# Performance work log

Measured on AMD Instinct MI355X. Metric: run time of the kernel, lower is better.

Reference implementation:

```python
import jax, jax.numpy as jnp
import numpy as np

KNN_K = 3  # module hard-codes top-3 farthest sememes (torch.sort descending)


def setup_inputs() -> dict:
    key = jax.random.key(0)
    k1, k2, k3 = jax.random.split(key, 3)
    V, H = 50257, 1024
    L, W, S = 256, 16, 32
    embedding = jax.random.normal(k1, (V, H), dtype=jnp.float32)
    word_ids = jax.random.randint(k2, (L, W), 0, V, dtype=jnp.int32)
    sememe_ids = jax.random.randint(k3, (L, W, S), 0, V, dtype=jnp.int32)
    return {"embedding": embedding, "word_ids": word_ids, "sememe_ids": sememe_ids}


def reference(embedding, word_ids, sememe_ids):
    # embedding: [V,H]; word_ids: [L,W]; sememe_ids: [L,W,S]
    w = embedding[word_ids]                  # [L,W,H]  word embeddings (s)
    sm = embedding[sememe_ids]               # [L,W,S,H] sememe embeddings
    # F.pairwise_distance(s, sememe_tensor, p=2): L2 per sememe
    dist = jnp.linalg.norm(sm - w[:, :, None, :], axis=-1)  # [L,W,S]
    # torch.sort(distance, descending=True)[1][:3] -> 3 farthest sememes
    _, idx = jax.lax.top_k(dist, KNN_K)                      # [L,W,K]
    sel = jnp.take_along_axis(sm, idx[..., None], axis=2)    # [L,W,K,H]
    # cat([knn_mean.unsqueeze(0), s], 0).mean(0) == (knn_mean + s) / 2
    per_word = 0.5 * (sel.mean(axis=2) + w)                  # [L,W,H]
    # stack(span).mean(0): mean over words in each label
    return per_word.mean(axis=1)                             # [L,H]
```

## Files before the change

### kernel.cpp

```cpp
#include <hip/hip_runtime.h>


#define HDIM 1024
#define SNUM 32
#define WNUM 16
#define KNN  3

__global__ __launch_bounds__(256) void knn_dist_kernel(
    const float* __restrict__ emb,
    const int*   __restrict__ word_ids,
    const int*   __restrict__ sem_ids,
    float*       __restrict__ dist_part,
    int nj)
{
    const int wave = threadIdx.x >> 6;
    const int lane = threadIdx.x & 63;
    const int blk  = blockIdx.x;
    const int b    = blk >> 2;
    const int quarter = blk & 3;

    const int base_s = b * SNUM + wave * 8;
    const int col    = quarter * 256 + 4 * lane;

    const int4 sa = *(const int4*)(sem_ids + base_s);
    const int4 sb = *(const int4*)(sem_ids + base_s + 4);
    const int  wid = word_ids[b];

    const float4 w = *(const float4*)(emb + (size_t)wid * HDIM + col);

    const int sids[8] = {sa.x, sa.y, sa.z, sa.w, sb.x, sb.y, sb.z, sb.w};
    float4 sv[8];
    #pragma unroll
    for (int k = 0; k < 8; ++k)
        sv[k] = *(const float4*)(emb + (size_t)sids[k] * HDIM + col);

    #pragma unroll
    for (int k = 0; k < 8; ++k) {
        const float dx = sv[k].x - w.x;
        const float dy = sv[k].y - w.y;
        const float dz = sv[k].z - w.z;
        const float dw = sv[k].w - w.w;
        float d = (dx * dx + dy * dy) + (dz * dz + dw * dw);
        #pragma unroll
        for (int off = 32; off >= 1; off >>= 1)
            d += __shfl_xor(d, off, 64);
        if (lane == 0)
            dist_part[(size_t)quarter * nj + base_s + k] = d;
    }
}

__global__ __launch_bounds__(256) void knn_select_kernel(
    const float* __restrict__ dist_part,
    const int*   __restrict__ word_ids,
    const int*   __restrict__ sem_ids,
    int*         __restrict__ sel,
    int nb, int nj)
{
    const int b = blockIdx.x * 256 + threadIdx.x;
    if (b >= nb) return;

    float4 acc[8];
    #pragma unroll
    for (int i = 0; i < 8; ++i) acc[i] = make_float4(0.f, 0.f, 0.f, 0.f);

    #pragma unroll
    for (int q = 0; q < 4; ++q) {
        const float4* p = (const float4*)(dist_part + (size_t)q * nj + b * SNUM);
        #pragma unroll
        for (int i = 0; i < 8; ++i) {
            const float4 v = p[i];
            acc[i].x += v.x; acc[i].y += v.y; acc[i].z += v.z; acc[i].w += v.w;
        }
    }

    float dl[SNUM];
    #pragma unroll
    for (int i = 0; i < 8; ++i) {
        dl[4 * i + 0] = acc[i].x;
        dl[4 * i + 1] = acc[i].y;
        dl[4 * i + 2] = acc[i].z;
        dl[4 * i + 3] = acc[i].w;
    }

    unsigned chosen = 0;
    #pragma unroll
    for (int k = 0; k < KNN; ++k) {
        float best = -1.0f;
        int   bi   = 0;
        #pragma unroll
        for (int s = 0; s < SNUM; ++s) {
            if (!((chosen >> s) & 1u) && dl[s] > best) { best = dl[s]; bi = s; }
        }
        chosen |= (1u << bi);
        sel[b * 4 + k] = sem_ids[b * SNUM + bi];
    }
    sel[b * 4 + 3] = word_ids[b];
}

__global__ __launch_bounds__(256) void knn_out_kernel(
    const float* __restrict__ emb,
    const int*   __restrict__ sel,
    float*       __restrict__ out)
{
    const int l = blockIdx.x >> 2;
    const int q = blockIdx.x & 3;
    const int h = q * 256 + threadIdx.x;

    __shared__ int s_ids[WNUM * 4];
    if (threadIdx.x < WNUM * 4) s_ids[threadIdx.x] = sel[l * WNUM * 4 + threadIdx.x];
    __syncthreads();

    const float third = 1.0f / 3.0f;
    float acc = 0.0f;
    #pragma unroll
    for (int w = 0; w < WNUM; ++w) {
        const float e0 = emb[(size_t)s_ids[w * 4 + 0] * HDIM + h];
        const float e1 = emb[(size_t)s_ids[w * 4 + 1] * HDIM + h];
        const float e2 = emb[(size_t)s_ids[w * 4 + 2] * HDIM + h];
        const float ew = emb[(size_t)s_ids[w * 4 + 3] * HDIM + h];
        acc += (e0 + e1 + e2) * third + ew;
    }
    out[(size_t)l * HDIM + h] = acc * (0.5f / 16.0f);
}

extern "C" void kernel_launch(void* const* d_in, const int* in_sizes, int n_in,
                              void* d_out, int out_size, void* d_ws, size_t ws_size,
                              hipStream_t stream) {
    const float* emb  = (const float*)d_in[0];
    const int*   wids = (const int*)d_in[1];
    const int*   sids = (const int*)d_in[2];
    float*       out  = (float*)d_out;

    const int nb = in_sizes[1];
    const int nj = in_sizes[2];
    const int L  = out_size / HDIM;

    float* dist_part = (float*)d_ws;
    int*   sel       = (int*)((char*)d_ws + (size_t)4 * nj * 4);

    knn_dist_kernel<<<dim3(nb * 4), dim3(256), 0, stream>>>(emb, wids, sids, dist_part, nj);
    knn_select_kernel<<<dim3((nb + 255) / 256), dim3(256), 0, stream>>>(dist_part, wids, sids, sel, nb, nj);
    knn_out_kernel<<<dim3(L * 4), dim3(256), 0, stream>>>(emb, sel, out);
}
```

Baseline: 91.57 us.

## Fuse top-k selection into output kernel and vectorize gathers and distance stores

Result: no change. 90.18 us (-1.5%).

```diff
diff --git a/kernel.cpp b/kernel.cpp
--- a/kernel.cpp
+++ b/kernel.cpp
@@ -19,14 +19,19 @@
     const int b    = blk >> 2;
     const int quarter = blk & 3;
 
+    __shared__ float s_w[256];
+
+    const int wid = word_ids[b];
+    s_w[threadIdx.x] = emb[(size_t)wid * HDIM + quarter * 256 + threadIdx.x];
+
     const int base_s = b * SNUM + wave * 8;
     const int col    = quarter * 256 + 4 * lane;
 
     const int4 sa = *(const int4*)(sem_ids + base_s);
     const int4 sb = *(const int4*)(sem_ids + base_s + 4);
-    const int  wid = word_ids[b];
 
-    const float4 w = *(const float4*)(emb + (size_t)wid * HDIM + col);
+    __syncthreads();
+    const float4 w = *(const float4*)(s_w + 4 * lane);
 
     const int sids[8] = {sa.x, sa.y, sa.z, sa.w, sb.x, sb.y, sb.z, sb.w};
     float4 sv[8];
@@ -34,93 +39,97 @@
     for (int k = 0; k < 8; ++k)
         sv[k] = *(const float4*)(emb + (size_t)sids[k] * HDIM + col);
 
+    float d[8];
     #pragma unroll
     for (int k = 0; k < 8; ++k) {
         const float dx = sv[k].x - w.x;
         const float dy = sv[k].y - w.y;
         const float dz = sv[k].z - w.z;
         const float dw = sv[k].w - w.w;
-        float d = (dx * dx + dy * dy) + (dz * dz + dw * dw);
+        d[k] = (dx * dx + dy * dy) + (dz * dz + dw * dw);
+    }
+
+    #pragma unroll
+    for (int k = 0; k < 8; ++k) {
         #pragma unroll
         for (int off = 32; off >= 1; off >>= 1)
-            d += __shfl_xor(d, off, 64);
-        if (lane == 0)
-            dist_part[(size_t)quarter * nj + base_s + k] = d;
+            d[k] += __shfl_xor(d[k], off, 64);
+    }
+
+    if (lane == 0) {
+        float* p = dist_part + (size_t)quarter * nj + base_s;
+        *(float4*)(p + 0) = make_float4(d[0], d[1], d[2], d[3]);
+        *(float4*)(p + 4) = make_float4(d[4], d[5], d[6], d[7]);
     }
 }
 
-__global__ __launch_bounds__(256) void knn_select_kernel(
+__global__ __launch_bounds__(256) void knn_outsel_kernel(
+    const float* __restrict__ emb,
     const float* __restrict__ dist_part,
     const int*   __restrict__ word_ids,
     const int*   __restrict__ sem_ids,
-    int*         __restrict__ sel,
-    int nb, int nj)
+    float*       __restrict__ out,
+    int nj)
 {
-    const int b = blockIdx.x * 256 + threadIdx.x;
-    if (b >= nb) return;
+    const int l = blockIdx.x;
+    const int t = threadIdx.x;
 
-    float4 acc[8];
-    #pragma unroll
-    for (int i = 0; i < 8; ++i) acc[i] = make_float4(0.f, 0.f, 0.f, 0.f);
+    __shared__ int s_ids[WNUM * 4];
 
-    #pragma unroll
-    for (int q = 0; q < 4; ++q) {
-        const float4* p = (const float4*)(dist_part + (size_t)q * nj + b * SNUM);
+    if (t < WNUM) {
+        const int b = l * WNUM + t;
+        float4 acc[8];
+        #pragma unroll
+        for (int i = 0; i < 8; ++i) acc[i] = make_float4(0.f, 0.f, 0.f, 0.f);
+        #pragma unroll
+        for (int q = 0; q < 4; ++q) {
+            const float4* p = (const float4*)(dist_part + (size_t)q * nj + b * SNUM);
+            #pragma unroll
+            for (int i = 0; i < 8; ++i) {
+                const float4 v = p[i];
+                acc[i].x += v.x; acc[i].y += v.y; acc[i].z += v.z; acc[i].w += v.w;
+            }
+        }
+        float dl[SNUM];
         #pragma unroll
         for (int i = 0; i < 8; ++i) {
-            const float4 v = p[i];
-            acc[i].x += v.x; acc[i].y += v.y; acc[i].z += v.z; acc[i].w += v.w;
+            dl[4 * i + 0] = acc[i].x;
+            dl[4 * i + 1] = acc[i].y;
+            dl[4 * i + 2] = acc[i].z;
+            dl[4 * i + 3] = acc[i].w;
         }
+        unsigned chosen = 0;
+        #pragma unroll
+        for (int k = 0; k < KNN; ++k) {
+            float best = -1.0f;
+            int   bi   = 0;
+            #pragma unroll
+            for (int s = 0; s < SNUM; ++s) {
+                if (!((chosen >> s) & 1u) && dl[s] > best) { best = dl[s]; bi = s; }
+            }
+            chosen |= (1u << bi);
+            s_ids[t * 4 + k] = sem_ids[b * SNUM + bi];
+        }
+        s_ids[t * 4 + 3] = word_ids[b];
     }
-
-    float dl[SNUM];
-    #pragma unroll
-    for (int i = 0; i < 8; ++i) {
-        dl[4 * i + 0] = acc[i].x;
-        dl[4 * i + 1] = acc[i].y;
-        dl[4 * i + 2] = acc[i].z;
-        dl[4 * i + 3] = acc[i].w;
-    }
-
-    unsigned chosen = 0;
-    #pragma unroll
-    for (int k = 0; k < KNN; ++k) {
-        float best = -1.0f;
-        int   bi   = 0;
-        #pragma unroll
-        for (int s = 0; s < SNUM; ++s) {
-            if (!((chosen >> s) & 1u) && dl[s] > best) { best = dl[s]; bi = s; }
-        }
-        chosen |= (1u << bi);
-        sel[b * 4 + k] = sem_ids[b * SNUM + bi];
-    }
-    sel[b * 4 + 3] = word_ids[b];
-}
-
-__global__ __launch_bounds__(256) void knn_out_kernel(
-    const float* __restrict__ emb,
-    const int*   __restrict__ sel,
-    float*       __restrict__ out)
-{
-    const int l = blockIdx.x >> 2;
-    const int q = blockIdx.x & 3;
-    const int h = q * 256 + threadIdx.x;
-
-    __shared__ int s_ids[WNUM * 4];
-    if (threadIdx.x < WNUM * 4) s_ids[threadIdx.x] = sel[l * WNUM * 4 + threadIdx.x];
     __syncthreads();
 
     const float third = 1.0f / 3.0f;
-    float acc = 0.0f;
-    #pragma unroll
+    float ax = 0.f, ay = 0.f, az = 0.f, aw = 0.f;
+    #pragma unroll 4
     for (int w = 0; w < WNUM; ++w) {
-        const float e0 = emb[(size_t)s_ids[w * 4 + 0] * HDIM + h];
-        const float e1 = emb[(size_t)s_ids[w * 4 + 1] * HDIM + h];
-        const float e2 = emb[(size_t)s_ids[w * 4 + 2] * HDIM + h];
-        const float ew = emb[(size_t)s_ids[w * 4 + 3] * HDIM + h];
-        acc += (e0 + e1 + e2) * third + ew;
+        const float4 e0 = *(const float4*)(emb + (size_t)s_ids[w * 4 + 0] * HDIM + 4 * t);
+        const float4 e1 = *(const float4*)(emb + (size_t)s_ids[w * 4 + 1] * HDIM + 4 * t);
+        const float4 e2 = *(const float4*)(emb + (size_t)s_ids[w * 4 + 2] * HDIM + 4 * t);
+        const float4 ew = *(const float4*)(emb + (size_t)s_ids[w * 4 + 3] * HDIM + 4 * t);
+        ax += (e0.x + e1.x + e2.x) * third + ew.x;
+        ay += (e0.y + e1.y + e2.y) * third + ew.y;
+        az += (e0.z + e1.z + e2.z) * third + ew.z;
+        aw += (e0.w + e1.w + e2.w) * third + ew.w;
     }
-    out[(size_t)l * HDIM + h] = acc * (0.5f / 16.0f);
+    const float scale = 0.5f / 16.0f;
+    *(float4*)(out + (size_t)l * HDIM + 4 * t) =
+        make_float4(ax * scale, ay * scale, az * scale, aw * scale);
 }
 
 extern "C" void kernel_launch(void* const* d_in, const int* in_sizes, int n_in,
@@ -136,9 +145,7 @@
     const int L  = out_size / HDIM;
 
     float* dist_part = (float*)d_ws;
-    int*   sel       = (int*)((char*)d_ws + (size_t)4 * nj * 4);
 
     knn_dist_kernel<<<dim3(nb * 4), dim3(256), 0, stream>>>(emb, wids, sids, dist_part, nj);
-    knn_select_kernel<<<dim3((nb + 255) / 256), dim3(256), 0, stream>>>(dist_part, wids, sids, sel, nb, nj);
-    knn_out_kernel<<<dim3(L * 4), dim3(256), 0, stream>>>(emb, sel, out);
+    knn_outsel_kernel<<<dim3(L), dim3(256), 0, stream>>>(emb, dist_part, wids, sids, out, nj);
 }
```
